# Kernel tuning notes

Hardware: AMD Instinct MI355X
Metric: run time of the kernel (lower is better)

The kernel has to match this reference:

```python
import jax, jax.numpy as jnp
import numpy as np

B = 512
V = 6890   # SMPL vertices
NJ = 24    # joints (global)
NB = 10    # shape betas
NP = 207   # pose blendshape features = 23*9
NJO = 19   # cocoplus output joints
PARENTS = np.array([0,0,0,0,1,2,3,4,5,6,7,8,9,9,9,12,13,14,16,17,18,19,20,21], dtype=np.int32)


def setup_inputs() -> dict:
    key = jax.random.key(0)
    ks = jax.random.split(key, 7)
    inputs = jax.random.normal(ks[0], (B, 82), jnp.float32) * 0.2  # [pose(72) | shape(10)]
    v_template = jax.random.normal(ks[1], (V, 3), jnp.float32)
    shapes = jax.random.normal(ks[2], (NB, V * 3), jnp.float32) * 0.01
    posedirs = jax.random.normal(ks[3], (NP, V * 3), jnp.float32) * 0.01
    jr = jax.random.uniform(ks[4], (V, NJ), jnp.float32)
    smpl_regressor = jr / jnp.sum(jr, axis=0, keepdims=True)          # columns sum to 1 over vertices
    w = jax.random.uniform(ks[5], (V, NJ), jnp.float32) ** 4
    lbs_weights = w / jnp.sum(w, axis=1, keepdims=True)               # rows sum to 1 over joints
    cr = jax.random.uniform(ks[6], (V, NJO), jnp.float32)
    joint_regressor = cr / jnp.sum(cr, axis=0, keepdims=True)
    parents = jnp.asarray(PARENTS)
    return {"inputs": inputs, "v_template": v_template, "shapes": shapes,
            "posedirs": posedirs, "smpl_regressor": smpl_regressor,
            "lbs_weights": lbs_weights, "joint_regressor": joint_regressor,
            "parents": parents}


def _rodrigues(pose):  # [B,72] -> [B,24,3,3]
    r = pose.reshape(-1, 3)
    angle = jnp.linalg.norm(r + 1e-8, axis=1, keepdims=True)  # [N,1]
    n = r / angle
    c = jnp.cos(angle)[:, :, None]   # [N,1,1]
    s = jnp.sin(angle)[:, :, None]
    outer = n[:, :, None] * n[:, None, :]
    z = jnp.zeros_like(n[:, 0])
    K = jnp.stack([z, -n[:, 2], n[:, 1],
                   n[:, 2], z, -n[:, 0],
                   -n[:, 1], n[:, 0], z], axis=1).reshape(-1, 3, 3)
    R = c * jnp.eye(3, dtype=pose.dtype) + (1.0 - c) * outer + s * K
    return R.reshape(-1, NJ, 3, 3)


def _make_A(R, t):  # R [B,3,3], t [B,3] -> [B,4,4]
    top = jnp.concatenate([R, t[:, :, None]], axis=2)
    bottom = jnp.broadcast_to(jnp.array([0., 0., 0., 1.], dtype=R.dtype), (R.shape[0], 1, 4))
    return jnp.concatenate([top, bottom], axis=1)


def _global_rigid(rotations, joints, parents_np):
    # sequential kinematic-chain composition over the fixed 24-joint tree
    res = [_make_A(rotations[:, 0], joints[:, 0])]
    for i in range(1, NJ):
        p = int(parents_np[i])
        t = joints[:, i] - joints[:, p]
        res.append(jnp.matmul(res[p], _make_A(rotations[:, i], t)))
    A_world = jnp.stack(res, axis=1)                 # [B,24,4,4]
    new_J = A_world[:, :, :3, 3]
    Jw0 = jnp.concatenate([joints, jnp.zeros(joints.shape[:2] + (1,), joints.dtype)], axis=2)[..., None]
    init_bone = jnp.matmul(A_world, Jw0)[..., 0]     # [B,24,4]
    pad = jnp.zeros_like(A_world).at[:, :, :, 3].set(init_bone)
    return new_J, A_world - pad


def reference(inputs, v_template, shapes, posedirs, smpl_regressor, lbs_weights, joint_regressor, parents):
    b = inputs.shape[0]
    pose = inputs[:, :72]
    beta = inputs[:, -10:]
    v_shaped = jnp.matmul(beta, shapes).reshape(b, V, 3) + v_template
    v_joints = jnp.einsum('bvc,vj->bjc', v_shaped, smpl_regressor)        # [B,24,3]
    rot = _rodrigues(pose)                                                # [B,24,3,3]
    pose_feature = (rot[:, 1:] - jnp.eye(3, dtype=rot.dtype)).reshape(b, -1)  # [B,207]
    v_posed = jnp.matmul(pose_feature, posedirs).reshape(b, V, 3) + v_shaped
    joint_transformed, A = _global_rigid(rot, v_joints, np.asarray(parents))
    T = jnp.einsum('vj,bjk->bvk', lbs_weights, A.reshape(b, NJ, 16)).reshape(b, V, 4, 4)
    v_homo = jnp.concatenate([v_posed, jnp.ones((b, V, 1), v_posed.dtype)], axis=2)
    vertices = jnp.einsum('bvij,bvj->bvi', T, v_homo)[:, :, :3]
    joints = jnp.einsum('bvc,vj->bjc', vertices, joint_regressor)         # [B,19,3]
    return vertices, joints, rot
```

## Files before the change

### kernel.cpp

```cpp
#include <hip/hip_runtime.h>

#define B_   512
#define V_   6890
#define NJ_  24
#define NB_  10
#define NP_  207
#define NJO_ 19



#define SRB_   192
#define SRCH_  862
#define RODB_  48
#define TRB_   26

__global__ void __launch_bounds__(256) k_pre(const float* __restrict__ in,
                                             const float* __restrict__ shapes,
                                             const float* __restrict__ vt,
                                             const float* __restrict__ sreg,
                                             const float* __restrict__ jreg,
                                             float* __restrict__ srtr,
                                             float* __restrict__ out_rot,
                                             float* __restrict__ pf_t,
                                             float* __restrict__ jreg_t,
                                             float* __restrict__ jout) {
  int blk = blockIdx.x;
  int tid = threadIdx.x;
  if (blk < SRB_) {
    int j  = blk >> 3;
    int ch = blk & 7;
    int vend = (ch + 1) * SRCH_; if (vend > V_) vend = V_;
    float acc[33];
#pragma unroll
    for (int a = 0; a < 33; a++) acc[a] = 0.f;
    for (int v = ch * SRCH_ + tid; v < vend; v += 256) {
      float w = sreg[v * NJ_ + j];
#pragma unroll
      for (int k = 0; k < NB_; k++) {
        const float* sp = shapes + k * (V_ * 3) + 3 * v;
#pragma unroll
        for (int c = 0; c < 3; c++) acc[k * 3 + c] += w * sp[c];
      }
#pragma unroll
      for (int c = 0; c < 3; c++) acc[30 + c] += w * vt[3 * v + c];
    }
    __shared__ float red[4][33];
    int wave = tid >> 6, lane = tid & 63;
#pragma unroll
    for (int a = 0; a < 33; a++) {
      float x = acc[a];
#pragma unroll
      for (int m = 1; m < 64; m <<= 1) x += __shfl_xor(x, m, 64);
      if (lane == 0) red[wave][a] = x;
    }
    __syncthreads();
    if (tid < 33) {
      float s = red[0][tid] + red[1][tid] + red[2][tid] + red[3][tid];
      if (tid < 30) atomicAdd(&srtr[((tid / 3) * NJ_ + j) * 3 + (tid % 3)], s);
      else          atomicAdd(&srtr[720 + j * 3 + (tid - 30)], s);
    }
  } else if (blk < SRB_ + RODB_) {
    int idx = (blk - SRB_) * 256 + tid;
    int b = idx & (B_ - 1);
    int j = idx >> 9;
    const float* r = in + b * 82 + j * 3;
    float r0 = r[0], r1 = r[1], r2 = r[2];
    float ax = r0 + 1e-8f, ay = r1 + 1e-8f, az = r2 + 1e-8f;
    float angle = sqrtf(ax * ax + ay * ay + az * az);
    float inv = 1.0f / angle;
    float n0 = r0 * inv, n1 = r1 * inv, n2 = r2 * inv;
    float c = cosf(angle), s = sinf(angle);
    float ic = 1.0f - c;
    float R[9];
    R[0] = c + ic * n0 * n0;      R[1] = ic * n0 * n1 - s * n2;  R[2] = ic * n0 * n2 + s * n1;
    R[3] = ic * n1 * n0 + s * n2; R[4] = c + ic * n1 * n1;       R[5] = ic * n1 * n2 - s * n0;
    R[6] = ic * n2 * n0 - s * n1; R[7] = ic * n2 * n1 + s * n0;  R[8] = c + ic * n2 * n2;
    float* ro = out_rot + b * 216 + j * 9;
#pragma unroll
    for (int q = 0; q < 9; q++) ro[q] = R[q];
    if (j > 0) {
#pragma unroll
      for (int q = 0; q < 9; q++)
        pf_t[(size_t)((j - 1) * 9 + q) * B_ + b] = R[q] - ((q % 4 == 0) ? 1.0f : 0.0f);
    }
  } else {
    int idx = (blk - SRB_ - RODB_) * 256 + tid;
    for (int q = idx; q < B_ * NJO_ * 3; q += TRB_ * 256) jout[q] = 0.f;
    for (int e = idx; e < V_ * NJO_; e += TRB_ * 256) {
      int jo = e / V_;
      int v  = e - jo * V_;
      jreg_t[e] = jreg[v * NJO_ + jo];
    }
  }
}

__global__ void __launch_bounds__(192) k_chain(const float* __restrict__ in,
                                               const float* __restrict__ rot,
                                               const float* __restrict__ srtr,
                                               const int* __restrict__ parents,
                                               float* __restrict__ Abuf) {
  (void)parents;
  constexpr int P[NJ_] = {0, 0, 0, 0, 1, 2, 3, 4, 5, 6, 7, 8, 9, 9, 9, 12, 13, 14,
                          16, 17, 18, 19, 20, 21};
  int tid = threadIdx.x;
  int bl = tid & 63;
  int r  = tid >> 6;
  int b  = blockIdx.x * 64 + bl;
  float beta[NB_];
#pragma unroll
  for (int k = 0; k < NB_; k++) beta[k] = in[b * 82 + 72 + k];
  float J[NJ_][3];
#pragma unroll
  for (int j = 0; j < NJ_; j++) {
#pragma unroll
    for (int c = 0; c < 3; c++) {
      float s = srtr[720 + j * 3 + c];
#pragma unroll
      for (int k = 0; k < NB_; k++) s += beta[k] * srtr[(k * NJ_ + j) * 3 + c];
      J[j][c] = s;
    }
  }
  const float* Rb = rot + b * 216;
  float A[NJ_][4];
#pragma unroll
  for (int c = 0; c < 3; c++) A[0][c] = Rb[r * 3 + c];
  A[0][3] = J[0][r];
#pragma unroll
  for (int j = 1; j < NJ_; j++) {
    const int p = P[j];
    float t0 = J[j][0] - J[p][0];
    float t1 = J[j][1] - J[p][1];
    float t2 = J[j][2] - J[p][2];
    float Rj[9];
#pragma unroll
    for (int q = 0; q < 9; q++) Rj[q] = Rb[j * 9 + q];
    float p0 = A[p][0], p1 = A[p][1], p2 = A[p][2], p3 = A[p][3];
#pragma unroll
    for (int c = 0; c < 3; c++)
      A[j][c] = p0 * Rj[c] + p1 * Rj[3 + c] + p2 * Rj[6 + c];
    A[j][3] = p0 * t0 + p1 * t1 + p2 * t2 + p3;
  }
  float* Ab = Abuf + (size_t)b * 288 + r * 4;
#pragma unroll
  for (int j = 0; j < NJ_; j++) {
    float4 o;
    o.x = A[j][0]; o.y = A[j][1]; o.z = A[j][2];
    o.w = A[j][3] - (A[j][0] * J[j][0] + A[j][1] * J[j][1] + A[j][2] * J[j][2]);
    *reinterpret_cast<float4*>(Ab + j * 12) = o;
  }
}

#define PB_ 8
#define BT_ 32
#define GX_ 108
#define GY_ 16
#define NWG_ (GX_ * GY_)
__global__ void __launch_bounds__(256) k_main(const float* __restrict__ in,
                                              const float* __restrict__ shapes,
                                              const float* __restrict__ vt,
                                              const float* __restrict__ posedirs,
                                              const float* __restrict__ lbs,
                                              const float* __restrict__ pf_t,
                                              const float* __restrict__ Abuf,
                                              float* __restrict__ verts) {
  __shared__ float lbs_l[64 * 25];
  int tid = threadIdx.x;
  int raw  = blockIdx.y * GX_ + blockIdx.x;
  int virt = (raw & 7) * (NWG_ / 8) + (raw >> 3);
  int vblk = virt >> 4;
  int bblk = virt & (GY_ - 1);
  int v0 = vblk * 64;
  int b0 = bblk * BT_;
  int nv = V_ - v0; if (nv > 64) nv = 64;
  for (int i = tid; i < nv * NJ_; i += 256)
    lbs_l[(i / NJ_) * 25 + (i % NJ_)] = lbs[(size_t)v0 * NJ_ + i];
  __syncthreads();
  int lane = tid & 63;
  int g = tid >> 6;
  int bb0 = __builtin_amdgcn_readfirstlane(b0 + g * PB_);
  int v = v0 + lane;
  int vc = v < V_ ? v : V_ - 1;

  float acc[PB_][3];
  {
    float t0 = vt[3 * vc + 0], t1 = vt[3 * vc + 1], t2 = vt[3 * vc + 2];
#pragma unroll
    for (int i = 0; i < PB_; i++) { acc[i][0] = t0; acc[i][1] = t1; acc[i][2] = t2; }
  }
#pragma unroll
  for (int k = 0; k < NB_; k++) {
    const float* sp = shapes + k * (V_ * 3) + 3 * vc;
    float s0 = sp[0], s1 = sp[1], s2 = sp[2];
#pragma unroll
    for (int i = 0; i < PB_; i++) {
      float bv = in[(size_t)(bb0 + i) * 82 + 72 + k];
      acc[i][0] += bv * s0; acc[i][1] += bv * s1; acc[i][2] += bv * s2;
    }
  }
  for (int p = 0; p < NP_; p++) {
    const float* pp = posedirs + (size_t)p * (V_ * 3) + 3 * vc;
    float d0 = pp[0], d1 = pp[1], d2 = pp[2];
    const float* pfp = pf_t + (size_t)p * B_ + bb0;
#pragma unroll
    for (int i = 0; i < PB_; i++) {
      float f = pfp[i];
      acc[i][0] += f * d0; acc[i][1] += f * d1; acc[i][2] += f * d2;
    }
  }
  float o[PB_][3];
#pragma unroll
  for (int i = 0; i < PB_; i++) { o[i][0] = 0.f; o[i][1] = 0.f; o[i][2] = 0.f; }
  for (int j = 0; j < NJ_; j++) {
    float w = lbs_l[lane * 25 + j];
#pragma unroll
    for (int i = 0; i < PB_; i++) {
      const float* M = Abuf + (size_t)(bb0 + i) * 288 + j * 12;
      float x = acc[i][0], y = acc[i][1], z = acc[i][2];
      o[i][0] += w * (M[0] * x + M[1] * y + M[2]  * z + M[3]);
      o[i][1] += w * (M[4] * x + M[5] * y + M[6]  * z + M[7]);
      o[i][2] += w * (M[8] * x + M[9] * y + M[10] * z + M[11]);
    }
  }
  if (v < V_) {
#pragma unroll
    for (int i = 0; i < PB_; i++) {
      float* op = verts + (size_t)(bb0 + i) * (V_ * 3) + 3 * v;
      op[0] = o[i][0]; op[1] = o[i][1]; op[2] = o[i][2];
    }
  }
}

#define JCH_ 1728
__global__ void __launch_bounds__(256) k_joints(const float* __restrict__ verts,
                                                const float* __restrict__ jreg_t,
                                                float* __restrict__ jout) {
  int b = blockIdx.x;
  int ch = blockIdx.y;
  int tid = threadIdx.x;
  int vend = (ch + 1) * JCH_; if (vend > V_) vend = V_;
  float acc[NJO_ * 3];
#pragma unroll
  for (int a = 0; a < NJO_ * 3; a++) acc[a] = 0.f;
  const float* vb = verts + (size_t)b * V_ * 3;
  for (int v = ch * JCH_ + tid; v < vend; v += 256) {
    float x = vb[3 * v + 0], y = vb[3 * v + 1], z = vb[3 * v + 2];
#pragma unroll
    for (int jo = 0; jo < NJO_; jo++) {
      float w = jreg_t[jo * V_ + v];
      acc[jo * 3 + 0] += w * x; acc[jo * 3 + 1] += w * y; acc[jo * 3 + 2] += w * z;
    }
  }
  __shared__ float red[4][NJO_ * 3];
  int wave = tid >> 6, lane = tid & 63;
#pragma unroll
  for (int a = 0; a < NJO_ * 3; a++) {
    float x = acc[a];
#pragma unroll
    for (int m = 1; m < 64; m <<= 1) x += __shfl_xor(x, m, 64);
    if (lane == 0) red[wave][a] = x;
  }
  __syncthreads();
  if (tid < NJO_ * 3) {
    float s = red[0][tid] + red[1][tid] + red[2][tid] + red[3][tid];
    atomicAdd(&jout[b * (NJO_ * 3) + tid], s);
  }
}

extern "C" void kernel_launch(void* const* d_in, const int* in_sizes, int n_in,
                              void* d_out, int out_size, void* d_ws, size_t ws_size,
                              hipStream_t stream) {
  const float* inputs   = (const float*)d_in[0];
  const float* v_templ  = (const float*)d_in[1];
  const float* shapes   = (const float*)d_in[2];
  const float* posedirs = (const float*)d_in[3];
  const float* sreg     = (const float*)d_in[4];
  const float* lbs      = (const float*)d_in[5];
  const float* jreg     = (const float*)d_in[6];
  const int*   parents  = (const int*)d_in[7];

  float* out   = (float*)d_out;
  float* verts = out;
  float* jout  = out + 10583040;
  float* rot   = out + 10612224;

  float* ws     = (float*)d_ws;
  float* pf_t   = ws;
  float* Abuf   = ws + 105984;
  float* srtr   = ws + 105984 + 147456;
  float* jreg_t = srtr + 792;

  hipMemsetAsync(srtr, 0, 792 * sizeof(float), stream);

  k_pre  <<<SRB_ + RODB_ + TRB_, 256, 0, stream>>>(inputs, shapes, v_templ, sreg, jreg,
                                                   srtr, rot, pf_t, jreg_t, jout);
  k_chain<<<8, 192, 0, stream>>>(inputs, rot, srtr, parents, Abuf);
  dim3 gmain(GX_, GY_);
  k_main <<<gmain, 256, 0, stream>>>(inputs, shapes, v_templ, posedirs, lbs, pf_t, Abuf, verts);
  dim3 gj(B_, 4);
  k_joints<<<gj, 256, 0, stream>>>(verts, jreg_t, jout);
}
```

Before: 266.8 us.

## Stage posedirs tiles through double-buffered LDS with coalesced loads

Measured after the change: 287.3 us. +7.7%, slower.

```diff
diff --git a/kernel.cpp b/kernel.cpp
--- a/kernel.cpp
+++ b/kernel.cpp
@@ -86,6 +86,7 @@
   } else {
     int idx = (blk - SRB_ - RODB_) * 256 + tid;
     for (int q = idx; q < B_ * NJO_ * 3; q += TRB_ * 256) jout[q] = 0.f;
+    if (idx < B_) pf_t[(size_t)NP_ * B_ + idx] = 0.f;
     for (int e = idx; e < V_ * NJO_; e += TRB_ * 256) {
       int jo = e / V_;
       int v  = e - jo * V_;
@@ -150,11 +151,14 @@
   }
 }
 
-#define PB_ 8
-#define BT_ 32
-#define GX_ 108
-#define GY_ 16
-#define NWG_ (GX_ * GY_)
+#define PB_   8
+#define BT_   32
+#define GX_   108
+#define GY_   16
+#define NWG_  (GX_ * GY_)
+#define TILE_ 8
+#define NT_   26
+#define ROWF_ 192
 __global__ void __launch_bounds__(256) k_main(const float* __restrict__ in,
                                               const float* __restrict__ shapes,
                                               const float* __restrict__ vt,
@@ -164,6 +168,7 @@
                                               const float* __restrict__ Abuf,
                                               float* __restrict__ verts) {
   __shared__ float lbs_l[64 * 25];
+  __shared__ float pd[2][TILE_ * ROWF_];
   int tid = threadIdx.x;
   int raw  = blockIdx.y * GX_ + blockIdx.x;
   int virt = (raw & 7) * (NWG_ / 8) + (raw >> 3);
@@ -174,13 +179,21 @@
   int nv = V_ - v0; if (nv > 64) nv = 64;
   for (int i = tid; i < nv * NJ_; i += 256)
     lbs_l[(i / NJ_) * 25 + (i % NJ_)] = lbs[(size_t)v0 * NJ_ + i];
-  __syncthreads();
   int lane = tid & 63;
   int g = tid >> 6;
   int bb0 = __builtin_amdgcn_readfirstlane(b0 + g * PB_);
   int v = v0 + lane;
   int vc = v < V_ ? v : V_ - 1;
 
+  int srow[6], scol[6];
+#pragma unroll
+  for (int q = 0; q < 6; q++) {
+    int idx = q * 256 + tid;
+    srow[q] = idx / ROWF_;
+    scol[q] = idx - srow[q] * ROWF_;
+  }
+  int ebase = 3 * v0;
+
   float acc[PB_][3];
   {
     float t0 = vt[3 * vc + 0], t1 = vt[3 * vc + 1], t2 = vt[3 * vc + 2];
@@ -197,15 +210,49 @@
       acc[i][0] += bv * s0; acc[i][1] += bv * s1; acc[i][2] += bv * s2;
     }
   }
-  for (int p = 0; p < NP_; p++) {
-    const float* pp = posedirs + (size_t)p * (V_ * 3) + 3 * vc;
-    float d0 = pp[0], d1 = pp[1], d2 = pp[2];
-    const float* pfp = pf_t + (size_t)p * B_ + bb0;
-#pragma unroll
-    for (int i = 0; i < PB_; i++) {
-      float f = pfp[i];
-      acc[i][0] += f * d0; acc[i][1] += f * d1; acc[i][2] += f * d2;
-    }
+  {
+    float stg[6];
+#pragma unroll
+    for (int q = 0; q < 6; q++) {
+      int rg = srow[q];
+      int off = ebase + scol[q]; if (off > V_ * 3 - 1) off = V_ * 3 - 1;
+      stg[q] = posedirs[(size_t)rg * (V_ * 3) + off];
+    }
+    __syncthreads();
+#pragma unroll
+    for (int q = 0; q < 6; q++) pd[0][q * 256 + tid] = stg[q];
+    __syncthreads();
+  }
+  for (int t = 0; t < NT_; t++) {
+    float stg[6];
+    const bool more = (t + 1 < NT_);
+    if (more) {
+#pragma unroll
+      for (int q = 0; q < 6; q++) {
+        int rg = (t + 1) * TILE_ + srow[q]; if (rg > NP_ - 1) rg = NP_ - 1;
+        int off = ebase + scol[q]; if (off > V_ * 3 - 1) off = V_ * 3 - 1;
+        stg[q] = posedirs[(size_t)rg * (V_ * 3) + off];
+      }
+    }
+    const float* pdb = pd[t & 1];
+#pragma unroll
+    for (int r = 0; r < TILE_; r++) {
+      float d0 = pdb[r * ROWF_ + 3 * lane + 0];
+      float d1 = pdb[r * ROWF_ + 3 * lane + 1];
+      float d2 = pdb[r * ROWF_ + 3 * lane + 2];
+      const float* pfp = pf_t + (size_t)(t * TILE_ + r) * B_ + bb0;
+#pragma unroll
+      for (int i = 0; i < PB_; i++) {
+        float f = pfp[i];
+        acc[i][0] += f * d0; acc[i][1] += f * d1; acc[i][2] += f * d2;
+      }
+    }
+    if (more) {
+      float* dst = pd[(t + 1) & 1];
+#pragma unroll
+      for (int q = 0; q < 6; q++) dst[q * 256 + tid] = stg[q];
+    }
+    __syncthreads();
   }
   float o[PB_][3];
 #pragma unroll
@@ -285,8 +332,8 @@
 
   float* ws     = (float*)d_ws;
   float* pf_t   = ws;
-  float* Abuf   = ws + 105984;
-  float* srtr   = ws + 105984 + 147456;
+  float* Abuf   = ws + 106496;
+  float* srtr   = ws + 106496 + 147456;
   float* jreg_t = srtr + 792;
 
   hipMemsetAsync(srtr, 0, 792 * sizeof(float), stream);
```
